# Kernel optimization log

Measured on AMD Instinct MI355X. Metric: run time of the kernel, lower is better.

## Reference

```python
import jax, jax.numpy as jnp
import numpy as np

# Dimensions
B, D, C, E = 4096, 1024, 512, 16            # batch, embedding_dim, context_dim, n_experts
LIN, R, LOUT = 1024, 16, 1024               # lora_dim = (in, r, out)
H_GATE, H_EXP, Z = 2048, 2048, 512          # gating hidden, expert hidden, expert out


def setup_inputs() -> dict:
    key = jax.random.key(0)
    ks = jax.random.split(key, 12)
    sc = 0.02
    return {
        "s": jax.random.normal(ks[0], (B, D), jnp.float32),
        "c": jax.random.normal(ks[1], (B, C), jnp.float32),
        # gating_model: Linear(D,2048) -> ReLU -> Linear(2048,E) -> Softmax
        "Wg1": jax.random.normal(ks[2], (D, H_GATE), jnp.float32) * sc,
        "bg1": jnp.zeros((H_GATE,), jnp.float32),
        "Wg2": jax.random.normal(ks[3], (H_GATE, E), jnp.float32) * sc,
        "bg2": jnp.zeros((E,), jnp.float32),
        # experts (stacked): Linear(D+C,2048) -> ReLU -> Linear(2048,512)
        "We1": jax.random.normal(ks[4], (E, D + C, H_EXP), jnp.float32) * sc,
        "be1": jnp.zeros((E, H_EXP), jnp.float32),
        "We2": jax.random.normal(ks[5], (E, H_EXP, Z), jnp.float32) * sc,
        "be2": jnp.zeros((E, Z), jnp.float32),
        # LoRA decode heads
        "WA": jax.random.normal(ks[6], (Z, LIN * R), jnp.float32) * sc,
        "bA": jnp.zeros((LIN * R,), jnp.float32),
        "WB": jax.random.normal(ks[7], (Z, R * LOUT), jnp.float32) * sc,
        "bB": jnp.zeros((R * LOUT,), jnp.float32),
    }


def reference(s, c, Wg1, bg1, Wg2, bg2, We1, be1, We2, be2, WA, bA, WB, bB):
    x = jnp.concatenate([s, c], axis=-1)                         # (B, D+C)
    # gating: softmax over experts
    gates = jax.nn.softmax(jnp.maximum(s @ Wg1 + bg1, 0.0) @ Wg2 + bg2, axis=-1)  # (B, E)
    # all-expert dense 2-layer MLPs (soft MoE)
    h = jnp.maximum(jnp.einsum('bd,edh->ebh', x, We1) + be1[:, None, :], 0.0)     # (E, B, H_EXP)
    eo = jnp.einsum('ebh,ehz->ebz', h, We2) + be2[:, None, :]                     # (E, B, Z)
    # gating-weighted sum over experts
    z = jnp.einsum('be,ebz->bz', gates, eo)                      # (B, Z)
    # LoRA decode heads, reshaped per batch element
    A = (z @ WA + bA).reshape(B, LIN, R)
    Bm = (z @ WB + bB).reshape(B, R, LOUT)
    return (A, Bm)
```

## Files before the change

### kernel.cpp

```cpp
#include <hip/hip_runtime.h>
#include <stdint.h>

typedef __attribute__((ext_vector_type(4))) float f32x4;
typedef __attribute__((ext_vector_type(8))) __bf16 bf16x8;

__device__ __forceinline__ ushort f2bf(float f) {
  union { float f; uint32_t u; } v; v.f = f;
  uint32_t r = v.u + 0x7fffu + ((v.u >> 16) & 1u);
  return (ushort)(r >> 16);
}
__device__ __forceinline__ float bf2f(uint32_t h) {
  union { uint32_t u; float f; } v; v.u = h << 16;
  return v.f;
}

__device__ __forceinline__ void gload16(const void* g, const void* l) {
  __builtin_amdgcn_global_load_lds(
      (const __attribute__((address_space(1))) void*)(uintptr_t)g,
      (__attribute__((address_space(3))) void*)(uint32_t)(uintptr_t)l,
      16, 0, 0);
}

template<int EPI, int COL>
__global__ __launch_bounds__(512, 1)
void gemm256p(const ushort* __restrict__ A, const ushort* __restrict__ Bt,
              const float* __restrict__ bias, const float* __restrict__ bias2,
              void* __restrict__ outp,
              int K, int lda, int ldb, int ldo,
              size_t aStride, size_t bStride, int biasStride, size_t oStride,
              const float* __restrict__ gates, int ebase)
{
  __shared__ __attribute__((aligned(16))) char smem[3 * 32768];

  const int bx = COL ? blockIdx.y : blockIdx.x;
  const int by = COL ? blockIdx.x : blockIdx.y;
  const int eb = blockIdx.z;

  const int t    = threadIdx.x;
  const int lane = t & 63;
  const int wid  = t >> 6;
  const int wr   = wid >> 2, wc = wid & 3;
  const int fr   = lane & 15, fq = lane >> 4;

  const int r  = t >> 2;
  const int jc = (t & 3) ^ ((t >> 3) & 3);
  const ushort* Ae = A  + aStride * eb;
  const ushort* Be = Bt + bStride * eb;
  const ushort* sA0 = Ae + (size_t)(by * 256 + (r >> 6) * 128 +   0 + (r & 63)) * lda + jc * 8;
  const ushort* sA1 = Ae + (size_t)(by * 256 + (r >> 6) * 128 +  64 + (r & 63)) * lda + jc * 8;
  const ushort* sB0 = Be + (size_t)(bx * 256 +   0 + r) * ldb + jc * 8;
  const ushort* sB1 = Be + (size_t)(bx * 256 + 128 + r) * ldb + jc * 8;
  const int dT = t * 16;

  const int swz  = (fq ^ ((fr >> 1) & 3)) * 16;
  const int aOff = (wr * 64 + fr) * 64 + swz;
  const int bOff = 16384 + (wc * 64 + fr) * 64 + swz;

  f32x4 acc[8][4];
#pragma unroll
  for (int m = 0; m < 8; ++m)
#pragma unroll
    for (int n = 0; n < 4; ++n) acc[m][n] = (f32x4){0.f, 0.f, 0.f, 0.f};

  const int NT = K >> 5;

#pragma unroll
  for (int kt = 0; kt < 2; ++kt) {
    char* d = smem + kt * 32768;
    gload16(sA0 + kt * 32, d + dT);
    gload16(sB0 + kt * 32, d + 16384 + dT);
    gload16(sB1 + kt * 32, d + 24576 + dT);
    gload16(sA1 + kt * 32, d + 8192 + dT);
  }

  int sc = 0;
  for (int T = 0; T < NT; ++T) {
    const char* base = smem + sc * 32768;
    const int ssi = (sc + 2 >= 3) ? sc - 1 : sc + 2;
    char* d = smem + ssi * 32768;
    const bool pf = (T + 2 < NT);
    const int ko = (T + 2) * 32;

    if (T < NT - 1) asm volatile("s_waitcnt vmcnt(5)" ::: "memory");
    else            asm volatile("s_waitcnt vmcnt(1)" ::: "memory");
    __builtin_amdgcn_s_barrier();
    if (pf) { gload16(sA0 + ko, d + dT); gload16(sB0 + ko, d + 16384 + dT); }

    bf16x8 af[4], bf[4];
#pragma unroll
    for (int m = 0; m < 4; ++m) af[m] = *(const bf16x8*)(base + aOff + m * 1024);
#pragma unroll
    for (int n = 0; n < 4; ++n) bf[n] = *(const bf16x8*)(base + bOff + n * 1024);
    __builtin_amdgcn_s_setprio(1);
#pragma unroll
    for (int m = 0; m < 4; ++m)
#pragma unroll
      for (int n = 0; n < 4; ++n)
        acc[m][n] = __builtin_amdgcn_mfma_f32_16x16x32_bf16(af[m], bf[n], acc[m][n], 0, 0, 0);
    __builtin_amdgcn_s_setprio(0);

    if (T < NT - 2)       asm volatile("s_waitcnt vmcnt(6)" ::: "memory");
    else if (T == NT - 2) asm volatile("s_waitcnt vmcnt(4)" ::: "memory");
    else                  asm volatile("s_waitcnt vmcnt(0)" ::: "memory");
    __builtin_amdgcn_s_barrier();
    if (pf) { gload16(sB1 + ko, d + 24576 + dT); gload16(sA1 + ko, d + 8192 + dT); }

#pragma unroll
    for (int m = 0; m < 4; ++m) af[m] = *(const bf16x8*)(base + 8192 + aOff + m * 1024);
    __builtin_amdgcn_s_setprio(1);
#pragma unroll
    for (int m = 0; m < 4; ++m)
#pragma unroll
      for (int n = 0; n < 4; ++n)
        acc[4 + m][n] = __builtin_amdgcn_mfma_f32_16x16x32_bf16(af[m], bf[n], acc[4 + m][n], 0, 0, 0);
    __builtin_amdgcn_s_setprio(0);

    sc = (sc + 1 == 3) ? 0 : sc + 1;
  }

  const int grow0 = by * 256 + wr * 128 + fq * 4;
  const int gcol0 = bx * 256 + wc * 64 + fr;

  if (EPI == 0) {
    ushort* oo = (ushort*)outp + oStride * eb;
    const float* bb = bias + (size_t)biasStride * eb;
#pragma unroll
    for (int n = 0; n < 4; ++n) {
      const int cc = gcol0 + n * 16;
      const float bv = bb[cc];
#pragma unroll
      for (int m = 0; m < 8; ++m) {
        const int rb = grow0 + (m >> 2) * 64 + (m & 3) * 16;
#pragma unroll
        for (int j = 0; j < 4; ++j) {
          const float v = acc[m][n][j] + bv;
          oo[(size_t)(rb + j) * ldo + cc] = f2bf(v > 0.f ? v : 0.f);
        }
      }
    }
  } else if (EPI == 1) {
    const int e = ebase + eb;
    float* oo = (float*)outp + oStride * e;
    const float* bb = bias + (size_t)biasStride * eb;
#pragma unroll
    for (int n = 0; n < 4; ++n) {
      const int cc = gcol0 + n * 16;
      const float bv = bb[cc];
#pragma unroll
      for (int m = 0; m < 8; ++m) {
        const int rb = grow0 + (m >> 2) * 64 + (m & 3) * 16;
#pragma unroll
        for (int j = 0; j < 4; ++j) {
          const int rr = rb + j;
          oo[(size_t)rr * ldo + cc] =
              gates[(size_t)rr * 16 + e] * (acc[m][n][j] + bv);
        }
      }
    }
  } else {
    const bool second = (gcol0 >= ldo);
    const float* bp = second ? bias2 : bias;
    float* oo = (float*)outp + (second ? oStride : 0);
#pragma unroll
    for (int n = 0; n < 4; ++n) {
      const int cc = gcol0 + n * 16 - (second ? ldo : 0);
      const float bv = bp[cc];
#pragma unroll
      for (int m = 0; m < 8; ++m) {
        const int rb = grow0 + (m >> 2) * 64 + (m & 3) * 16;
#pragma unroll
        for (int j = 0; j < 4; ++j)
          oo[(size_t)(rb + j) * ldo + cc] = acc[m][n][j] + bv;
      }
    }
  }
}

__global__ __launch_bounds__(256)
void transpose_cvt(const float* __restrict__ in, ushort* __restrict__ out,
                   int K, int N, size_t inStride, size_t outStride)
{
  __shared__ float tile[64][65];
  const float* I = in + inStride * blockIdx.z;
  ushort* O = out + outStride * blockIdx.z;
  const int n0 = blockIdx.x * 64, k0 = blockIdx.y * 64;
  const int t = threadIdx.x;
  const int r = t >> 4, cv = (t & 15) * 4;
#pragma unroll
  for (int pp = 0; pp < 4; ++pp) {
    const int kr = r + pp * 16;
    const float4 v = *(const float4*)&I[(size_t)(k0 + kr) * N + (n0 + cv)];
    tile[kr][cv] = v.x; tile[kr][cv + 1] = v.y; tile[kr][cv + 2] = v.z; tile[kr][cv + 3] = v.w;
  }
  __syncthreads();
#pragma unroll
  for (int pp = 0; pp < 4; ++pp) {
    const int nr = r + pp * 16;
    ushort4 o4;
    o4.x = f2bf(tile[cv + 0][nr]); o4.y = f2bf(tile[cv + 1][nr]);
    o4.z = f2bf(tile[cv + 2][nr]); o4.w = f2bf(tile[cv + 3][nr]);
    *(ushort4*)&O[(size_t)(n0 + nr) * K + (k0 + cv)] = o4;
  }
}

__global__ __launch_bounds__(256)
void build_x(const float* __restrict__ s, const float* __restrict__ c, ushort* __restrict__ x)
{
  const size_t i = (size_t)blockIdx.x * 256 + threadIdx.x;
  const size_t b = i / 192;
  const int col  = (int)(i % 192) * 8;
  const float* src = (col < 1024) ? (s + b * 1024 + col) : (c + b * 512 + (col - 1024));
  const float4 v0 = ((const float4*)src)[0];
  const float4 v1 = ((const float4*)src)[1];
  uint4 o;
  o.x = f2bf(v0.x) | ((uint32_t)f2bf(v0.y) << 16);
  o.y = f2bf(v0.z) | ((uint32_t)f2bf(v0.w) << 16);
  o.z = f2bf(v1.x) | ((uint32_t)f2bf(v1.y) << 16);
  o.w = f2bf(v1.z) | ((uint32_t)f2bf(v1.w) << 16);
  *(uint4*)(x + i * 8) = o;
}

__global__ __launch_bounds__(256)
void reduce_z(const float* __restrict__ zp, ushort* __restrict__ zb)
{
  const size_t i = ((size_t)blockIdx.x * 256 + threadIdx.x) * 4;
  const size_t S = (size_t)4096 * 512;
  float4 sv = {0.f, 0.f, 0.f, 0.f};
#pragma unroll
  for (int e = 0; e < 16; ++e) {
    const float4 v = *(const float4*)(zp + (size_t)e * S + i);
    sv.x += v.x; sv.y += v.y; sv.z += v.z; sv.w += v.w;
  }
  ushort4 o4;
  o4.x = f2bf(sv.x); o4.y = f2bf(sv.y); o4.z = f2bf(sv.z); o4.w = f2bf(sv.w);
  *(ushort4*)(zb + i) = o4;
}

__global__ __launch_bounds__(256)
void gating2_softmax(const ushort* __restrict__ hg, const float* __restrict__ Wg2,
                     const float* __restrict__ bg2, float* __restrict__ gates)
{
  const int row  = (int)((blockIdx.x * 256 + threadIdx.x) >> 6);
  const int lane = threadIdx.x & 63;
  float acc[16];
#pragma unroll
  for (int e = 0; e < 16; ++e) acc[e] = 0.f;
  const ushort* hrow = hg + (size_t)row * 2048;
#pragma unroll
  for (int it = 0; it < 4; ++it) {
    const int kb = it * 512 + lane * 8;
    const uint4 pk = *(const uint4*)(hrow + kb);
    float hv[8] = { bf2f(pk.x & 0xffffu), bf2f(pk.x >> 16),
                    bf2f(pk.y & 0xffffu), bf2f(pk.y >> 16),
                    bf2f(pk.z & 0xffffu), bf2f(pk.z >> 16),
                    bf2f(pk.w & 0xffffu), bf2f(pk.w >> 16) };
#pragma unroll
    for (int j = 0; j < 8; ++j) {
      const float* wrow = Wg2 + (size_t)(kb + j) * 16;
#pragma unroll
      for (int e = 0; e < 16; ++e) acc[e] += hv[j] * wrow[e];
    }
  }
#pragma unroll
  for (int e = 0; e < 16; ++e) {
#pragma unroll
    for (int off = 32; off > 0; off >>= 1) acc[e] += __shfl_xor(acc[e], off);
    acc[e] += bg2[e];
  }
  float mx = acc[0];
#pragma unroll
  for (int e = 1; e < 16; ++e) mx = fmaxf(mx, acc[e]);
  float sum = 0.f;
#pragma unroll
  for (int e = 0; e < 16; ++e) { acc[e] = __expf(acc[e] - mx); sum += acc[e]; }
  const float inv = 1.f / sum;
  if (lane == 0) {
#pragma unroll
    for (int e = 0; e < 16; ++e) gates[(size_t)row * 16 + e] = acc[e] * inv;
  }
}

extern "C" void kernel_launch(void* const* d_in, const int* in_sizes, int n_in,
                              void* d_out, int out_size, void* d_ws, size_t ws_size,
                              hipStream_t stream)
{
  (void)in_sizes; (void)n_in; (void)out_size;
  const float* s   = (const float*)d_in[0];
  const float* c   = (const float*)d_in[1];
  const float* Wg1 = (const float*)d_in[2];
  const float* bg1 = (const float*)d_in[3];
  const float* Wg2 = (const float*)d_in[4];
  const float* bg2 = (const float*)d_in[5];
  const float* We1 = (const float*)d_in[6];
  const float* be1 = (const float*)d_in[7];
  const float* We2 = (const float*)d_in[8];
  const float* be2 = (const float*)d_in[9];
  const float* WA  = (const float*)d_in[10];
  const float* bA  = (const float*)d_in[11];
  const float* WB  = (const float*)d_in[12];
  const float* bB  = (const float*)d_in[13];
  float* out = (float*)d_out;

  char* ws = (char*)d_ws;
  size_t off = 0;
  auto alloc = [&](size_t bytes) {
    void* p = ws + off; off += (bytes + 255) & ~(size_t)255; return p;
  };
  ushort* x     = (ushort*)alloc((size_t)4096 * 1536 * 2);
  ushort* We1T  = (ushort*)alloc((size_t)16 * 2048 * 1536 * 2);
  ushort* We2T  = (ushort*)alloc((size_t)16 * 512 * 2048 * 2);
  ushort* WABT  = (ushort*)alloc((size_t)32768 * 512 * 2);
  float*  gates = (float*)alloc((size_t)4096 * 16 * 4);
  float*  zp    = (float*)alloc((size_t)16 * 4096 * 512 * 4);
  ushort* zb    = (ushort*)alloc((size_t)4096 * 512 * 2);

  const size_t BH = (size_t)4096 * 2048 * 2;
  size_t rem = (ws_size > off) ? ws_size - off : 0;
  int GS = 2;
  if (rem >= 16 * BH) GS = 16;
  else if (rem >= 8 * BH) GS = 8;
  else if (rem >= 4 * BH) GS = 4;
  ushort* h = (ushort*)alloc((size_t)GS * BH);
  ushort* Wg1T = h;
  ushort* hg   = (ushort*)((char*)h + (size_t)2048 * 1024 * 2);

  const size_t S_We1 = (size_t)2048 * 1536;
  const size_t S_We2 = (size_t)512 * 2048;
  const size_t S_h   = (size_t)4096 * 2048;
  const size_t S_z   = (size_t)4096 * 512;

  build_x<<<3072, 256, 0, stream>>>(s, c, x);
  transpose_cvt<<<dim3(32, 16, 1),  256, 0, stream>>>(Wg1, Wg1T, 1024, 2048, 0, 0);
  transpose_cvt<<<dim3(32, 24, 16), 256, 0, stream>>>(We1, We1T, 1536, 2048, S_We1, S_We1);
  transpose_cvt<<<dim3(8, 32, 16),  256, 0, stream>>>(We2, We2T, 2048, 512, S_We2, S_We2);
  transpose_cvt<<<dim3(256, 8, 1),  256, 0, stream>>>(WA, WABT, 512, 16384, 0, 0);
  transpose_cvt<<<dim3(256, 8, 1),  256, 0, stream>>>(WB, WABT + (size_t)16384 * 512, 512, 16384, 0, 0);

  gemm256p<0, 1><<<dim3(16, 8, 1), 512, 0, stream>>>(x, Wg1T, bg1, nullptr, hg,
      1024, 1536, 1024, 2048, 0, 0, 0, 0, nullptr, 0);
  gating2_softmax<<<1024, 256, 0, stream>>>(hg, Wg2, bg2, gates);

  for (int g = 0; g < 16; g += GS) {
    gemm256p<0, 1><<<dim3(16, 8, GS), 512, 0, stream>>>(x, We1T + (size_t)g * S_We1,
        be1 + (size_t)g * 2048, nullptr, h,
        1536, 1536, 1536, 2048, 0, S_We1, 2048, S_h, nullptr, 0);
    gemm256p<1, 0><<<dim3(2, 16, GS), 512, 0, stream>>>(h, We2T + (size_t)g * S_We2,
        be2 + (size_t)g * 512, nullptr, zp,
        2048, 2048, 2048, 512, S_h, S_We2, 512, S_z, gates, g);
  }

  reduce_z<<<2048, 256, 0, stream>>>(zp, zb);

  gemm256p<3, 1><<<dim3(16, 128, 1), 512, 0, stream>>>(zb, WABT, bA, bB, out,
      512, 512, 512, 16384, 0, 0, 0, (size_t)4096 * 16384, nullptr, 0);
}
```

Measured before the change: 1.158 ms.

## Fold gates into expert hidden, concat experts along K, split-K second GEMM

The gate weight is folded into the first expert GEMM's epilogue: ReLU output is scaled by the gate and stored as bf16 into one wide h buffer laid out as (B, 16*2048). The second layer then becomes a single GEMM over the concatenated K=32768, split into 8 K-chunks, followed by a reduction that also adds the gate-weighted be2 bias. This removes the per-expert fp32 zp write of 16x(4096x512) and the grouped loop. The main loop is also rescheduled so LDS fragment reads and the next prefetch are issued before the barrier, with adjusted vmcnt waits. The cost is a larger h workspace and the risk that the tighter wait counts are wrong.

```diff
diff --git a/kernel.cpp b/kernel.cpp
--- a/kernel.cpp
+++ b/kernel.cpp
@@ -28,7 +28,7 @@
               void* __restrict__ outp,
               int K, int lda, int ldb, int ldo,
               size_t aStride, size_t bStride, int biasStride, size_t oStride,
-              const float* __restrict__ gates, int ebase)
+              const float* __restrict__ gates)
 {
   __shared__ __attribute__((aligned(16))) char smem[3 * 32768];
 
@@ -72,6 +72,8 @@
     gload16(sB1 + kt * 32, d + 24576 + dT);
     gload16(sA1 + kt * 32, d + 8192 + dT);
   }
+  asm volatile("s_waitcnt vmcnt(5)" ::: "memory");
+  __builtin_amdgcn_s_barrier();
 
   int sc = 0;
   for (int T = 0; T < NT; ++T) {
@@ -81,38 +83,39 @@
     const bool pf = (T + 2 < NT);
     const int ko = (T + 2) * 32;
 
-    if (T < NT - 1) asm volatile("s_waitcnt vmcnt(5)" ::: "memory");
-    else            asm volatile("s_waitcnt vmcnt(1)" ::: "memory");
+    if (T < NT - 1) asm volatile("s_waitcnt vmcnt(4)" ::: "memory");
+    else            asm volatile("s_waitcnt vmcnt(0)" ::: "memory");
+    bf16x8 afA[4], bfv[4];
+#pragma unroll
+    for (int m = 0; m < 4; ++m) afA[m] = *(const bf16x8*)(base + aOff + m * 1024);
+#pragma unroll
+    for (int n = 0; n < 4; ++n) bfv[n] = *(const bf16x8*)(base + bOff + n * 1024);
+    if (pf) { gload16(sA0 + ko, d + dT); gload16(sB0 + ko, d + 16384 + dT); }
+    __builtin_amdgcn_sched_barrier(0);
     __builtin_amdgcn_s_barrier();
-    if (pf) { gload16(sA0 + ko, d + dT); gload16(sB0 + ko, d + 16384 + dT); }
-
-    bf16x8 af[4], bf[4];
-#pragma unroll
-    for (int m = 0; m < 4; ++m) af[m] = *(const bf16x8*)(base + aOff + m * 1024);
-#pragma unroll
-    for (int n = 0; n < 4; ++n) bf[n] = *(const bf16x8*)(base + bOff + n * 1024);
     __builtin_amdgcn_s_setprio(1);
 #pragma unroll
     for (int m = 0; m < 4; ++m)
 #pragma unroll
       for (int n = 0; n < 4; ++n)
-        acc[m][n] = __builtin_amdgcn_mfma_f32_16x16x32_bf16(af[m], bf[n], acc[m][n], 0, 0, 0);
+        acc[m][n] = __builtin_amdgcn_mfma_f32_16x16x32_bf16(afA[m], bfv[n], acc[m][n], 0, 0, 0);
     __builtin_amdgcn_s_setprio(0);
 
-    if (T < NT - 2)       asm volatile("s_waitcnt vmcnt(6)" ::: "memory");
-    else if (T == NT - 2) asm volatile("s_waitcnt vmcnt(4)" ::: "memory");
+    if (T < NT - 2)       asm volatile("s_waitcnt vmcnt(3)" ::: "memory");
+    else if (T == NT - 2) asm volatile("s_waitcnt vmcnt(1)" ::: "memory");
     else                  asm volatile("s_waitcnt vmcnt(0)" ::: "memory");
+    bf16x8 afB[4];
+#pragma unroll
+    for (int m = 0; m < 4; ++m) afB[m] = *(const bf16x8*)(base + 8192 + aOff + m * 1024);
+    if (pf) { gload16(sB1 + ko, d + 24576 + dT); gload16(sA1 + ko, d + 8192 + dT); }
+    __builtin_amdgcn_sched_barrier(0);
     __builtin_amdgcn_s_barrier();
-    if (pf) { gload16(sB1 + ko, d + 24576 + dT); gload16(sA1 + ko, d + 8192 + dT); }
-
-#pragma unroll
-    for (int m = 0; m < 4; ++m) af[m] = *(const bf16x8*)(base + 8192 + aOff + m * 1024);
     __builtin_amdgcn_s_setprio(1);
 #pragma unroll
     for (int m = 0; m < 4; ++m)
 #pragma unroll
       for (int n = 0; n < 4; ++n)
-        acc[4 + m][n] = __builtin_amdgcn_mfma_f32_16x16x32_bf16(af[m], bf[n], acc[4 + m][n], 0, 0, 0);
+        acc[4 + m][n] = __builtin_amdgcn_mfma_f32_16x16x32_bf16(afB[m], bfv[n], acc[4 + m][n], 0, 0, 0);
     __builtin_amdgcn_s_setprio(0);
 
     sc = (sc + 1 == 3) ? 0 : sc + 1;
@@ -138,10 +141,16 @@
         }
       }
     }
-  } else if (EPI == 1) {
-    const int e = ebase + eb;
-    float* oo = (float*)outp + oStride * e;
+  } else if (EPI == 2) {
+    ushort* oo = (ushort*)outp + oStride * eb;
     const float* bb = bias + (size_t)biasStride * eb;
+    float gv[8][4];
+#pragma unroll
+    for (int m = 0; m < 8; ++m) {
+      const int rb = grow0 + (m >> 2) * 64 + (m & 3) * 16;
+#pragma unroll
+      for (int j = 0; j < 4; ++j) gv[m][j] = gates[(size_t)(rb + j) * 16 + eb];
+    }
 #pragma unroll
     for (int n = 0; n < 4; ++n) {
       const int cc = gcol0 + n * 16;
@@ -151,10 +160,22 @@
         const int rb = grow0 + (m >> 2) * 64 + (m & 3) * 16;
 #pragma unroll
         for (int j = 0; j < 4; ++j) {
-          const int rr = rb + j;
-          oo[(size_t)rr * ldo + cc] =
-              gates[(size_t)rr * 16 + e] * (acc[m][n][j] + bv);
+          const float v = acc[m][n][j] + bv;
+          oo[(size_t)(rb + j) * ldo + cc] = f2bf(v > 0.f ? gv[m][j] * v : 0.f);
         }
+      }
+    }
+  } else if (EPI == 4) {
+    float* oo = (float*)outp + oStride * eb;
+#pragma unroll
+    for (int n = 0; n < 4; ++n) {
+      const int cc = gcol0 + n * 16;
+#pragma unroll
+      for (int m = 0; m < 8; ++m) {
+        const int rb = grow0 + (m >> 2) * 64 + (m & 3) * 16;
+#pragma unroll
+        for (int j = 0; j < 4; ++j)
+          oo[(size_t)(rb + j) * ldo + cc] = acc[m][n][j];
       }
     }
   } else {
@@ -221,15 +242,24 @@
 }
 
 __global__ __launch_bounds__(256)
-void reduce_z(const float* __restrict__ zp, ushort* __restrict__ zb)
+void reduce_z8(const float* __restrict__ zs, const float* __restrict__ gates,
+               const float* __restrict__ be2, ushort* __restrict__ zb)
 {
   const size_t i = ((size_t)blockIdx.x * 256 + threadIdx.x) * 4;
   const size_t S = (size_t)4096 * 512;
+  const int rrow = (int)(i >> 9);
+  const int ccol = (int)(i & 511);
   float4 sv = {0.f, 0.f, 0.f, 0.f};
 #pragma unroll
+  for (int p = 0; p < 8; ++p) {
+    const float4 v = *(const float4*)(zs + (size_t)p * S + i);
+    sv.x += v.x; sv.y += v.y; sv.z += v.z; sv.w += v.w;
+  }
+#pragma unroll
   for (int e = 0; e < 16; ++e) {
-    const float4 v = *(const float4*)(zp + (size_t)e * S + i);
-    sv.x += v.x; sv.y += v.y; sv.z += v.z; sv.w += v.w;
+    const float ge = gates[(size_t)rrow * 16 + e];
+    const float4 bv = *(const float4*)(be2 + (size_t)e * 512 + ccol);
+    sv.x += ge * bv.x; sv.y += ge * bv.y; sv.z += ge * bv.z; sv.w += ge * bv.w;
   }
   ushort4 o4;
   o4.x = f2bf(sv.x); o4.y = f2bf(sv.y); o4.z = f2bf(sv.z); o4.w = f2bf(sv.w);
@@ -284,7 +314,7 @@
                               void* d_out, int out_size, void* d_ws, size_t ws_size,
                               hipStream_t stream)
 {
-  (void)in_sizes; (void)n_in; (void)out_size;
+  (void)in_sizes; (void)n_in; (void)out_size; (void)ws_size;
   const float* s   = (const float*)d_in[0];
   const float* c   = (const float*)d_in[1];
   const float* Wg1 = (const float*)d_in[2];
@@ -306,51 +336,40 @@
   auto alloc = [&](size_t bytes) {
     void* p = ws + off; off += (bytes + 255) & ~(size_t)255; return p;
   };
-  ushort* x     = (ushort*)alloc((size_t)4096 * 1536 * 2);
-  ushort* We1T  = (ushort*)alloc((size_t)16 * 2048 * 1536 * 2);
-  ushort* We2T  = (ushort*)alloc((size_t)16 * 512 * 2048 * 2);
-  ushort* WABT  = (ushort*)alloc((size_t)32768 * 512 * 2);
-  float*  gates = (float*)alloc((size_t)4096 * 16 * 4);
-  float*  zp    = (float*)alloc((size_t)16 * 4096 * 512 * 4);
-  ushort* zb    = (ushort*)alloc((size_t)4096 * 512 * 2);
-
-  const size_t BH = (size_t)4096 * 2048 * 2;
-  size_t rem = (ws_size > off) ? ws_size - off : 0;
-  int GS = 2;
-  if (rem >= 16 * BH) GS = 16;
-  else if (rem >= 8 * BH) GS = 8;
-  else if (rem >= 4 * BH) GS = 4;
-  ushort* h = (ushort*)alloc((size_t)GS * BH);
+  ushort* x      = (ushort*)alloc((size_t)4096 * 1536 * 2);
+  ushort* We1T   = (ushort*)alloc((size_t)16 * 2048 * 1536 * 2);
+  ushort* We2cat = (ushort*)alloc((size_t)512 * 32768 * 2);
+  ushort* WABT   = (ushort*)alloc((size_t)32768 * 512 * 2);
+  float*  gates  = (float*)alloc((size_t)4096 * 16 * 4);
+  float*  zsplit = (float*)alloc((size_t)8 * 4096 * 512 * 4);
+  ushort* zb     = (ushort*)alloc((size_t)4096 * 512 * 2);
+  ushort* h      = (ushort*)alloc((size_t)4096 * 32768 * 2);
   ushort* Wg1T = h;
   ushort* hg   = (ushort*)((char*)h + (size_t)2048 * 1024 * 2);
 
   const size_t S_We1 = (size_t)2048 * 1536;
   const size_t S_We2 = (size_t)512 * 2048;
-  const size_t S_h   = (size_t)4096 * 2048;
   const size_t S_z   = (size_t)4096 * 512;
 
   build_x<<<3072, 256, 0, stream>>>(s, c, x);
   transpose_cvt<<<dim3(32, 16, 1),  256, 0, stream>>>(Wg1, Wg1T, 1024, 2048, 0, 0);
   transpose_cvt<<<dim3(32, 24, 16), 256, 0, stream>>>(We1, We1T, 1536, 2048, S_We1, S_We1);
-  transpose_cvt<<<dim3(8, 32, 16),  256, 0, stream>>>(We2, We2T, 2048, 512, S_We2, S_We2);
+  transpose_cvt<<<dim3(8, 32, 16),  256, 0, stream>>>(We2, We2cat, 32768, 512, S_We2, 2048);
   transpose_cvt<<<dim3(256, 8, 1),  256, 0, stream>>>(WA, WABT, 512, 16384, 0, 0);
   transpose_cvt<<<dim3(256, 8, 1),  256, 0, stream>>>(WB, WABT + (size_t)16384 * 512, 512, 16384, 0, 0);
 
   gemm256p<0, 1><<<dim3(16, 8, 1), 512, 0, stream>>>(x, Wg1T, bg1, nullptr, hg,
-      1024, 1536, 1024, 2048, 0, 0, 0, 0, nullptr, 0);
+      1024, 1536, 1024, 2048, 0, 0, 0, 0, nullptr);
   gating2_softmax<<<1024, 256, 0, stream>>>(hg, Wg2, bg2, gates);
 
-  for (int g = 0; g < 16; g += GS) {
-    gemm256p<0, 1><<<dim3(16, 8, GS), 512, 0, stream>>>(x, We1T + (size_t)g * S_We1,
-        be1 + (size_t)g * 2048, nullptr, h,
-        1536, 1536, 1536, 2048, 0, S_We1, 2048, S_h, nullptr, 0);
-    gemm256p<1, 0><<<dim3(2, 16, GS), 512, 0, stream>>>(h, We2T + (size_t)g * S_We2,
-        be2 + (size_t)g * 512, nullptr, zp,
-        2048, 2048, 2048, 512, S_h, S_We2, 512, S_z, gates, g);
-  }
-
-  reduce_z<<<2048, 256, 0, stream>>>(zp, zb);
+  gemm256p<2, 1><<<dim3(16, 8, 16), 512, 0, stream>>>(x, We1T, be1, nullptr, h,
+      1536, 1536, 1536, 32768, 0, S_We1, 2048, 2048, gates);
+
+  gemm256p<4, 0><<<dim3(2, 16, 8), 512, 0, stream>>>(h, We2cat, be2, nullptr, zsplit,
+      4096, 32768, 32768, 512, 4096, 4096, 0, S_z, nullptr);
+
+  reduce_z8<<<2048, 256, 0, stream>>>(zsplit, gates, be2, zb);
 
   gemm256p<3, 1><<<dim3(16, 128, 1), 512, 0, stream>>>(zb, WABT, bA, bB, out,
-      512, 512, 512, 16384, 0, 0, 0, (size_t)4096 * 16384, nullptr, 0);
-}
+      512, 512, 512, 16384, 0, 0, 0, (size_t)4096 * 16384, nullptr);
+}
```

Measured after the change: 1.181 ms. Within noise of the previous version (+1.9%).
